# Kernel tuning notes

Hardware: AMD Instinct MI355X
Metric: run time of the kernel (lower is better)

Reference implementation:

```python
import jax, jax.numpy as jnp
import numpy as np
import math

BLKQ = 64
BLKK = 32
TOPK_FRAC = 0.1


def setup_inputs() -> dict:
    key = jax.random.key(0)
    k1, k2, k3, k4, k5 = jax.random.split(key, 5)
    B, L, H, D = 1, 8192, 16, 64
    q = jax.random.normal(k1, (B, L, H, D), jnp.float32)
    k = jax.random.normal(k2, (B, L, H, D), jnp.float32)
    v = jax.random.normal(k3, (B, L, H, D), jnp.float32)
    # proj_l initialized with nn.init.normal_ (std=1) in the original
    W_proj = jax.random.normal(k4, (D, D), jnp.float32)
    b_proj = jax.random.normal(k5, (D,), jnp.float32)
    return {"q": q, "k": k, "v": v, "W_proj": W_proj, "b_proj": b_proj}


def reference(q, k, v, W_proj, b_proj):
    B, L, H, D = q.shape
    lcm = BLKQ * BLKK // math.gcd(BLKQ, BLKK)
    L_pad = ((L + lcm - 1) // lcm) * lcm
    pad = L_pad - L
    scale = 1.0 / math.sqrt(D)

    # [B, L, H, D] -> [B, H, L_pad, D], zero padded (fused_transpose_pad)
    qt = jnp.transpose(q, (0, 2, 1, 3))
    kt = jnp.transpose(k, (0, 2, 1, 3))
    vt = jnp.transpose(v, (0, 2, 1, 3))
    if pad:
        pw = ((0, 0), (0, 0), (0, pad), (0, 0))
        qt_p = jnp.pad(qt, pw); kt_p = jnp.pad(kt, pw); vt_p = jnp.pad(vt, pw)
    else:
        qt_p, kt_p, vt_p = qt, kt, vt

    # key smoothing (SAGE): subtract per-(b,h) mean of padded k
    km = kt_p.mean(axis=-2, keepdims=True)          # [B, H, 1, D]
    kc = kt_p - km

    M = L_pad // BLKQ
    N = L_pad // BLKK
    # block pooling for routing scores
    pooled_q = qt_p.reshape(B, H, M, BLKQ, D).mean(axis=3)   # [B,H,M,D]
    pooled_k = kc.reshape(B, H, N, BLKK, D).mean(axis=3)     # [B,H,N,D]
    score = jnp.einsum('bhmd,bhnd->bhmn', pooled_q, pooled_k)

    T = min(N, int(TOPK_FRAC * N))                  # real_topk (static)
    _, idx = jax.lax.top_k(score, T)                # [B,H,M,T]
    lut = jnp.sort(idx, axis=-1)

    # gather selected key/value blocks: [B,H,M,T,BLKK,D]
    kb = kc.reshape(B, H, N, BLKK, D)
    vb = vt_p.reshape(B, H, N, BLKK, D)
    kg = jnp.take_along_axis(kb[:, :, None], lut[..., None, None], axis=3)
    vg = jnp.take_along_axis(vb[:, :, None], lut[..., None, None], axis=3)

    qb = qt_p.reshape(B, H, M, BLKQ, D)
    # block-sparse scores: [B,H,M,BLKQ,T,BLKK]
    s = jnp.einsum('bhmqd,bhmtkd->bhmqtk', qb, kg) * scale
    key_pos = lut[..., None] * BLKK + jnp.arange(BLKK)       # [B,H,M,T,BLKK]
    valid = key_pos < L
    s = jnp.where(valid[:, :, :, None, :, :], s, -jnp.inf)
    s = s.reshape(B, H, M, BLKQ, T * BLKK)
    p = jax.nn.softmax(s, axis=-1)
    o_s = jnp.einsum('bhmqn,bhmnd->bhmqd', p, vg.reshape(B, H, M, T * BLKK, D))
    o_s = o_s.reshape(B, H, L_pad, D)[:, :, :L]              # slice to seq_len

    # linear attention branch (softmax feature map over D)
    q_fm = jax.nn.softmax(qt_p[:, :, :L], axis=-1)
    k_fm = jax.nn.softmax(kt_p[:, :, :L], axis=-1)
    kvsum = jnp.einsum('bhld,bhle->bhde', k_fm, vt)          # [B,H,D,D]
    ksum = k_fm.sum(axis=-2)                                 # [B,H,D]
    denom = jnp.einsum('bhld,bhd->bhl', q_fm, ksum)[..., None] + 1e-6
    o_l = jnp.einsum('bhld,bhde->bhle', q_fm, kvsum) / denom
    o_l = o_l @ W_proj.T + b_proj                            # proj_l

    o = jnp.transpose(o_l + o_s, (0, 2, 1, 3))               # [B,L,H,D]
    return o
```

## Files before the change

### kernel.cpp

```cpp
#include <hip/hip_runtime.h>
#include <math.h>

#define SEQL 8192
#define NH 16
#define HD 1024
#define TSEL 25

#define OFF_KVPART 0
#define OFF_KSUM   262144
#define OFF_ZEND   263168
#define OFF_PK     263168
#define OFF_KWT    525312
#define OFF_KSWZ   558080

typedef __attribute__((ext_vector_type(8))) short bf16x8;
typedef __attribute__((ext_vector_type(4))) float f32x4;
typedef __attribute__((ext_vector_type(4))) unsigned u32x4;
typedef __attribute__((ext_vector_type(2))) unsigned u32x2;

static __device__ inline short f2bf(float f) {
    union { float f; unsigned u; } c; c.f = f;
    unsigned r = (c.u + 0x7FFFu + ((c.u >> 16) & 1u)) >> 16;
    return (short)r;
}
static __device__ inline bf16x8 cvt8(float4 a, float4 b) {
    bf16x8 r;
    r[0] = f2bf(a.x); r[1] = f2bf(a.y); r[2] = f2bf(a.z); r[3] = f2bf(a.w);
    r[4] = f2bf(b.x); r[5] = f2bf(b.y); r[6] = f2bf(b.z); r[7] = f2bf(b.w);
    return r;
}
static __device__ inline unsigned cvtpk(float a, float b) {
    unsigned r;
    asm("v_cvt_pk_bf16_f32 %0, %1, %2" : "=v"(r) : "v"(a), "v"(b));
    return r;
}
static __device__ inline float exp2a(float x) {
#if __has_builtin(__builtin_amdgcn_exp2f)
    return __builtin_amdgcn_exp2f(x);
#else
    float r; asm("v_exp_f32 %0, %1" : "=v"(r) : "v"(x)); return r;
#endif
}
#if __has_builtin(__builtin_amdgcn_permlane32_swap)
static __device__ inline unsigned xor32v(unsigned x, bool hi) {
    u32x2 r;
    {
        auto t = __builtin_amdgcn_permlane32_swap(x, x, false, false);
        r[0] = t[0]; r[1] = t[1];
    }
    return hi ? r[0] : r[1];
}
static __device__ inline unsigned xor16v(unsigned x, bool hi) {
    u32x2 r;
    {
        auto t = __builtin_amdgcn_permlane16_swap(x, x, false, false);
        r[0] = t[0]; r[1] = t[1];
    }
    return hi ? r[0] : r[1];
}
#else
static __device__ inline unsigned xor32v(unsigned x, bool hi) {
    unsigned a = x, b;
    asm("v_mov_b32 %0, %1" : "=v"(b) : "v"(x));
    asm("v_permlane32_swap_b32 %0, %1" : "+v"(a), "+v"(b));
    return hi ? a : b;
}
static __device__ inline unsigned xor16v(unsigned x, bool hi) {
    unsigned a = x, b;
    asm("v_mov_b32 %0, %1" : "=v"(b) : "v"(x));
    asm("v_permlane16_swap_b32 %0, %1" : "+v"(a), "+v"(b));
    return hi ? a : b;
}
#endif
static __device__ inline void load_lds16(const void* g, void* l) {
    __builtin_amdgcn_global_load_lds((const __attribute__((address_space(1))) unsigned int*)g,
                                     (__attribute__((address_space(3))) unsigned int*)l,
                                     16, 0, 0);
}

__global__ __launch_bounds__(256) void prep_lin(const float* __restrict__ k,
                                                const float* __restrict__ v,
                                                short* __restrict__ kswz,
                                                short* __restrict__ vswz,
                                                float* __restrict__ pk,
                                                float* __restrict__ kvpart,
                                                float* __restrict__ ksum) {
    __shared__ __align__(16) float kf[64][68];
    __shared__ __align__(16) float vv[64][68];
    __shared__ float pcol[2][4][64];
    int b = blockIdx.x;
    int h = b >> 6, sc = b & 63;
    int t = threadIdx.x;
    int lane = t & 63, w = t >> 6;
    int r32 = t >> 3, ch = t & 7;
    int d0 = (lane >> 4) * 4 + w * 16;
    int e0 = (lane & 15) * 4;
    float acc[16];
    #pragma unroll
    for (int i = 0; i < 16; i++) acc[i] = 0.f;
    float ks_acc = 0.f;

    const float* kb_ = k + (size_t)(sc * 128 + r32) * HD + h * 64 + ch * 8;
    const float* vb_ = v + (size_t)(sc * 128 + r32) * HD + h * 64 + ch * 8;
    float4 K0a = *(const float4*)kb_;
    float4 K0b = *(const float4*)(kb_ + 4);
    float4 K1a = *(const float4*)(kb_ + (size_t)32 * HD);
    float4 K1b = *(const float4*)(kb_ + (size_t)32 * HD + 4);
    float4 V0a = *(const float4*)vb_;
    float4 V0b = *(const float4*)(vb_ + 4);
    float4 V1a = *(const float4*)(vb_ + (size_t)32 * HD);
    float4 V1b = *(const float4*)(vb_ + (size_t)32 * HD + 4);

    #pragma unroll
    for (int ph = 0; ph < 2; ph++) {
        int n0 = sc * 4 + ph * 2;
        {
            *(float4*)&vv[r32][ch * 8]          = V0a;
            *(float4*)&vv[r32][ch * 8 + 4]      = V0b;
            *(float4*)&vv[32 + r32][ch * 8]     = V1a;
            *(float4*)&vv[32 + r32][ch * 8 + 4] = V1b;
        }
        {
            int f = r32 * 8 + (ch ^ (r32 & 7));
            *(bf16x8*)(kswz + (size_t)(h * 256 + n0) * 2048 + f * 8)     = cvt8(K0a, K0b);
            *(bf16x8*)(kswz + (size_t)(h * 256 + n0 + 1) * 2048 + f * 8) = cvt8(K1a, K1b);
        }
        {
            float s_[8] = { K0a.x, K0a.y, K0a.z, K0a.w, K0b.x, K0b.y, K0b.z, K0b.w };
            #pragma unroll
            for (int j = 0; j < 8; j++) {
                s_[j] += __shfl_xor(s_[j], 8, 64);
                s_[j] += __shfl_xor(s_[j], 16, 64);
                s_[j] += __shfl_xor(s_[j], 32, 64);
            }
            if (lane < 8) {
                #pragma unroll
                for (int j = 0; j < 8; j++) pcol[0][w][(t & 7) * 8 + j] = s_[j];
            }
            float s1_[8] = { K1a.x, K1a.y, K1a.z, K1a.w, K1b.x, K1b.y, K1b.z, K1b.w };
            #pragma unroll
            for (int j = 0; j < 8; j++) {
                s1_[j] += __shfl_xor(s1_[j], 8, 64);
                s1_[j] += __shfl_xor(s1_[j], 16, 64);
                s1_[j] += __shfl_xor(s1_[j], 32, 64);
            }
            if (lane < 8) {
                #pragma unroll
                for (int j = 0; j < 8; j++) pcol[1][w][(t & 7) * 8 + j] = s1_[j];
            }
        }
        {
            float mx = fmaxf(fmaxf(fmaxf(K0a.x, K0a.y), fmaxf(K0a.z, K0a.w)),
                             fmaxf(fmaxf(K0b.x, K0b.y), fmaxf(K0b.z, K0b.w)));
            mx = fmaxf(mx, __shfl_xor(mx, 1, 64));
            mx = fmaxf(mx, __shfl_xor(mx, 2, 64));
            mx = fmaxf(mx, __shfl_xor(mx, 4, 64));
            float4 Fa, Fb;
            Fa.x = __expf(K0a.x - mx); Fa.y = __expf(K0a.y - mx);
            Fa.z = __expf(K0a.z - mx); Fa.w = __expf(K0a.w - mx);
            Fb.x = __expf(K0b.x - mx); Fb.y = __expf(K0b.y - mx);
            Fb.z = __expf(K0b.z - mx); Fb.w = __expf(K0b.w - mx);
            float sm = (Fa.x + Fa.y + Fa.z + Fa.w) + (Fb.x + Fb.y + Fb.z + Fb.w);
            sm += __shfl_xor(sm, 1, 64);
            sm += __shfl_xor(sm, 2, 64);
            sm += __shfl_xor(sm, 4, 64);
            float inv = 1.f / sm;
            Fa.x *= inv; Fa.y *= inv; Fa.z *= inv; Fa.w *= inv;
            Fb.x *= inv; Fb.y *= inv; Fb.z *= inv; Fb.w *= inv;
            *(float4*)&kf[r32][ch * 8]     = Fa;
            *(float4*)&kf[r32][ch * 8 + 4] = Fb;
        }
        {
            float mx = fmaxf(fmaxf(fmaxf(K1a.x, K1a.y), fmaxf(K1a.z, K1a.w)),
                             fmaxf(fmaxf(K1b.x, K1b.y), fmaxf(K1b.z, K1b.w)));
            mx = fmaxf(mx, __shfl_xor(mx, 1, 64));
            mx = fmaxf(mx, __shfl_xor(mx, 2, 64));
            mx = fmaxf(mx, __shfl_xor(mx, 4, 64));
            float4 Fa, Fb;
            Fa.x = __expf(K1a.x - mx); Fa.y = __expf(K1a.y - mx);
            Fa.z = __expf(K1a.z - mx); Fa.w = __expf(K1a.w - mx);
            Fb.x = __expf(K1b.x - mx); Fb.y = __expf(K1b.y - mx);
            Fb.z = __expf(K1b.z - mx); Fb.w = __expf(K1b.w - mx);
            float sm = (Fa.x + Fa.y + Fa.z + Fa.w) + (Fb.x + Fb.y + Fb.z + Fb.w);
            sm += __shfl_xor(sm, 1, 64);
            sm += __shfl_xor(sm, 2, 64);
            sm += __shfl_xor(sm, 4, 64);
            float inv = 1.f / sm;
            Fa.x *= inv; Fa.y *= inv; Fa.z *= inv; Fa.w *= inv;
            Fb.x *= inv; Fb.y *= inv; Fb.z *= inv; Fb.w *= inv;
            *(float4*)&kf[32 + r32][ch * 8]     = Fa;
            *(float4*)&kf[32 + r32][ch * 8 + 4] = Fb;
        }
        if (ph < 1) {
            const float* kn = kb_ + (size_t)64 * HD;
            const float* vn = vb_ + (size_t)64 * HD;
            K0a = *(const float4*)kn;
            K0b = *(const float4*)(kn + 4);
            K1a = *(const float4*)(kn + (size_t)32 * HD);
            K1b = *(const float4*)(kn + (size_t)32 * HD + 4);
            V0a = *(const float4*)vn;
            V0b = *(const float4*)(vn + 4);
            V1a = *(const float4*)(vn + (size_t)32 * HD);
            V1b = *(const float4*)(vn + (size_t)32 * HD + 4);
        }
        __syncthreads();
        if (t < 128) {
            int s = t >> 6, d = t & 63;
            pk[(size_t)(h * 256 + n0 + s) * 64 + d] =
                (pcol[s][0][d] + pcol[s][1][d] + pcol[s][2][d] + pcol[s][3][d])
                * (1.f / 32.f);
        }
        {
            int c = w, d = lane;
            #pragma unroll
            for (int s = 0; s < 2; s++) {
                bf16x8 val;
                #pragma unroll
                for (int j = 0; j < 8; j++) val[j] = f2bf(vv[s * 32 + c * 8 + j][d]);
                int f = d * 4 + (c ^ ((d >> 1) & 3));
                *(bf16x8*)(vswz + (size_t)(h * 256 + n0 + s) * 2048 + f * 8) = val;
            }
        }
        #pragma unroll 8
        for (int l = 0; l < 64; l++) {
            float4 kd = *(const float4*)&kf[l][d0];
            float4 ve = *(const float4*)&vv[l][e0];
            acc[0]  += kd.x * ve.x; acc[1]  += kd.x * ve.y; acc[2]  += kd.x * ve.z; acc[3]  += kd.x * ve.w;
            acc[4]  += kd.y * ve.x; acc[5]  += kd.y * ve.y; acc[6]  += kd.y * ve.z; acc[7]  += kd.y * ve.w;
            acc[8]  += kd.z * ve.x; acc[9]  += kd.z * ve.y; acc[10] += kd.z * ve.z; acc[11] += kd.z * ve.w;
            acc[12] += kd.w * ve.x; acc[13] += kd.w * ve.y; acc[14] += kd.w * ve.z; acc[15] += kd.w * ve.w;
        }
        if (t < 64) {
            float s = 0.f;
            #pragma unroll 8
            for (int l = 0; l < 64; l++) s += kf[l][t];
            ks_acc += s;
        }
        __syncthreads();
    }
    float* dst = kvpart + ((size_t)(sc & 3) * 16 + h) * 4096;
    #pragma unroll
    for (int i = 0; i < 4; i++)
        #pragma unroll
        for (int j = 0; j < 4; j++)
            atomicAdd(&dst[(d0 + i) * 64 + e0 + j], acc[i * 4 + j]);
    if (t < 64) atomicAdd(&ksum[h * 64 + t], ks_acc);
}

__global__ __launch_bounds__(256) void kw_mul(const float* __restrict__ kvpart,
                                              const float* __restrict__ W,
                                              short* __restrict__ kwt) {
    __shared__ __align__(16) float kv[16][68];
    __shared__ __align__(16) float wsm[64][68];
    int h = blockIdx.x >> 2, dq = blockIdx.x & 3;
    int t = threadIdx.x;
    for (int i = t; i < 1024; i += 256) {
        int dl = i >> 6, e = i & 63;
        float s = 0.f;
        #pragma unroll
        for (int p = 0; p < 4; p++)
            s += kvpart[((size_t)p * 16 + h) * 4096 + (dq * 16 + dl) * 64 + e];
        kv[dl][e] = s;
    }
    for (int i = t; i < 4096; i += 256) wsm[i >> 6][i & 63] = W[i];
    __syncthreads();
    int lane = t & 63, wi = t >> 6;
    int dl = lane & 15;
    int db = wi * 16 + (lane >> 4) * 4;
    #pragma unroll
    for (int j = 0; j < 4; j++) {
        int dd = db + j;
        float a = 0.f;
        #pragma unroll
        for (int e4 = 0; e4 < 16; e4++) {
            float4 kq = *(const float4*)&kv[dl][e4 * 4];
            float4 wq = *(const float4*)&wsm[dd][e4 * 4];
            a += kq.x * wq.x + kq.y * wq.y + kq.z * wq.z + kq.w * wq.w;
        }
        kwt[(size_t)h * 4096 + dd * 64 + dq * 16 + dl] = f2bf(a);
    }
}

__global__ __launch_bounds__(256) void sparse_attn_mfma(const float* __restrict__ q,
                                                        const short* __restrict__ kswz,
                                                        const short* __restrict__ vswz,
                                                        const float* __restrict__ pk,
                                                        const short* __restrict__ kwt,
                                                        const float* __restrict__ ksum,
                                                        const float* __restrict__ bproj,
                                                        float* __restrict__ out) {
    __shared__ __align__(16) short Kb[3][2048];
    __shared__ __align__(16) short Vb[3][2048];
    __shared__ __align__(16) float pq_s[64];
    __shared__ __align__(16) float s_s[256];
    __shared__ int wcnt[4];
    __shared__ int lut_s[TSEL];

    int b = blockIdx.x;
    int x = b & 7, jj = b >> 3;
    int h = x * 2 + (jj >> 7);
    int m = jj & 127;
    int t = threadIdx.x;
    int lane = t & 63, w = t >> 6;
    int l15 = lane & 15, quad = lane >> 4;
    const bool b16 = (t & 16) != 0;
    const bool b32 = (t & 32) != 0;
    const bool beq = (b16 == b32);

    {
        load_lds16(kwt + (size_t)h * 4096 + t * 8, &Kb[1][t * 8]);
        load_lds16(kwt + (size_t)h * 4096 + 2048 + t * 8, &Vb[1][t * 8]);
    }

    if (t < 64) {
        const float* base = q + (size_t)m * 64 * HD + h * 64 + t;
        float s = 0.f;
        #pragma unroll 8
        for (int r = 0; r < 64; r++) s += base[(size_t)r * HD];
        pq_s[t] = s * (1.f / 64.f);
    }
    __syncthreads();
    {
        const float* kr = pk + ((size_t)h * 256 + t) * 64;
        double acc = 0.0;
        #pragma unroll 8
        for (int d = 0; d < 64; d++) acc += (double)pq_s[d] * (double)kr[d];
        float sc_ = (float)acc;
        s_s[t] = sc_;
        __syncthreads();
        int cnt = 0;
        float si = sc_;
        #pragma unroll 4
        for (int j4 = 0; j4 < 64; j4++) {
            float4 sv = *(const float4*)&s_s[j4 * 4];
            int j = j4 * 4;
            cnt += (sv.x > si) || (sv.x == si && (j + 0) < t);
            cnt += (sv.y > si) || (sv.y == si && (j + 1) < t);
            cnt += (sv.z > si) || (sv.z == si && (j + 2) < t);
            cnt += (sv.w > si) || (sv.w == si && (j + 3) < t);
        }
        bool sel = cnt < TSEL;
        unsigned long long bal = __ballot(sel);
        if (lane == 0) wcnt[w] = __popcll(bal);
        __syncthreads();
        if (sel) {
            int off = __popcll(bal & ((1ull << lane) - 1ull));
            for (int i = 0; i < w; i++) off += wcnt[i];
            lut_s[off] = t;
        }
        __syncthreads();
    }

    {
        size_t base = (size_t)(h * 256 + lut_s[0]) * 2048;
        load_lds16(kswz + base + t * 8, &Kb[0][t * 8]);
        load_lds16(vswz + base + t * 8, &Vb[0][t * 8]);
    }

    const float* qrow = q + (size_t)(m * 64 + w * 16 + l15) * HD + h * 64;
    float4 x0 = *(const float4*)(qrow + quad * 8);
    float4 x1 = *(const float4*)(qrow + quad * 8 + 4);
    float4 x2 = *(const float4*)(qrow + 32 + quad * 8);
    float4 x3 = *(const float4*)(qrow + 32 + quad * 8 + 4);
    bf16x8 qa[2];
    qa[0] = cvt8(x0, x1);
    qa[1] = cvt8(x2, x3);

    float mx = fmaxf(fmaxf(fmaxf(x0.x, x0.y), fmaxf(x0.z, x0.w)),
                     fmaxf(fmaxf(x1.x, x1.y), fmaxf(x1.z, x1.w)));
    mx = fmaxf(mx, fmaxf(fmaxf(fmaxf(x2.x, x2.y), fmaxf(x2.z, x2.w)),
                         fmaxf(fmaxf(x3.x, x3.y), fmaxf(x3.z, x3.w))));
    mx = fmaxf(mx, __shfl_xor(mx, 16, 64));
    mx = fmaxf(mx, __shfl_xor(mx, 32, 64));
    x0.x = __expf(x0.x - mx); x0.y = __expf(x0.y - mx); x0.z = __expf(x0.z - mx); x0.w = __expf(x0.w - mx);
    x1.x = __expf(x1.x - mx); x1.y = __expf(x1.y - mx); x1.z = __expf(x1.z - mx); x1.w = __expf(x1.w - mx);
    x2.x = __expf(x2.x - mx); x2.y = __expf(x2.y - mx); x2.z = __expf(x2.z - mx); x2.w = __expf(x2.w - mx);
    x3.x = __expf(x3.x - mx); x3.y = __expf(x3.y - mx); x3.z = __expf(x3.z - mx); x3.w = __expf(x3.w - mx);
    float sm = (x0.x + x0.y + x0.z + x0.w) + (x1.x + x1.y + x1.z + x1.w)
             + (x2.x + x2.y + x2.z + x2.w) + (x3.x + x3.y + x3.z + x3.w);
    sm += __shfl_xor(sm, 16, 64);
    sm += __shfl_xor(sm, 32, 64);
    float qsc = 1.f / sm;
    float4 ka0 = *(const float4*)(ksum + h * 64 + quad * 8);
    float4 ka1 = *(const float4*)(ksum + h * 64 + quad * 8 + 4);
    float4 ka2 = *(const float4*)(ksum + h * 64 + 32 + quad * 8);
    float4 ka3 = *(const float4*)(ksum + h * 64 + 32 + quad * 8 + 4);
    float dq = x0.x * ka0.x + x0.y * ka0.y + x0.z * ka0.z + x0.w * ka0.w
             + x1.x * ka1.x + x1.y * ka1.y + x1.z * ka1.z + x1.w * ka1.w
             + x2.x * ka2.x + x2.y * ka2.y + x2.z * ka2.z + x2.w * ka2.w
             + x3.x * ka3.x + x3.y * ka3.y + x3.z * ka3.z + x3.w * ka3.w;
    dq += __shfl_xor(dq, 16, 64);
    dq += __shfl_xor(dq, 32, 64);
    float invd = 1.f / (dq * qsc + 1e-6f);
    x0.x *= qsc; x0.y *= qsc; x0.z *= qsc; x0.w *= qsc;
    x1.x *= qsc; x1.y *= qsc; x1.z *= qsc; x1.w *= qsc;
    x2.x *= qsc; x2.y *= qsc; x2.z *= qsc; x2.w *= qsc;
    x3.x *= qsc; x3.y *= qsc; x3.z *= qsc; x3.w *= qsc;
    bf16x8 qf[2];
    qf[0] = cvt8(x0, x1);
    qf[1] = cvt8(x2, x3);

    __syncthreads();

    f32x4 Ol[4];
    #pragma unroll
    for (int dt = 0; dt < 4; dt++) Ol[dt] = (f32x4){0.f, 0.f, 0.f, 0.f};
    __builtin_amdgcn_s_setprio(1);
    #pragma unroll
    for (int dt = 0; dt < 4; dt++) {
        #pragma unroll
        for (int kc = 0; kc < 2; kc++) {
            int flat = (dt * 16 + l15) * 64 + kc * 32 + quad * 8;
            bf16x8 a = (dt < 2) ? *(const bf16x8*)&Kb[1][flat]
                                : *(const bf16x8*)&Vb[1][flat - 2048];
            Ol[dt] = __builtin_amdgcn_mfma_f32_16x16x32_bf16(a, qf[kc], Ol[dt], 0, 0, 0);
        }
    }
    __builtin_amdgcn_s_setprio(0);

    __syncthreads();
    {
        size_t base = (size_t)(h * 256 + lut_s[1]) * 2048;
        load_lds16(kswz + base + t * 8, &Kb[1][t * 8]);
        load_lds16(vswz + base + t * 8, &Vb[1][t * 8]);
    }

    f32x4 O[4];
    #pragma unroll
    for (int dt = 0; dt < 4; dt++) O[dt] = (f32x4){0.f, 0.f, 0.f, 0.f};
    float l_loc = 0.f;
    const f32x4 z = (f32x4){0.f, 0.f, 0.f, 0.f};
    const float EC = 1.44269504f * 0.125f;

    int bc = 0;
    for (int ti = 0; ti < TSEL; ti++) {
        if (ti > 0) {
            if (ti < TSEL - 1) asm volatile("s_waitcnt vmcnt(2)" ::: "memory");
            else               asm volatile("s_waitcnt vmcnt(0)" ::: "memory");
            __builtin_amdgcn_s_barrier();
            __builtin_amdgcn_sched_barrier(0);
        }
        if (ti + 2 < TSEL) {
            int bs = bc ? bc - 1 : 2;
            size_t base = (size_t)(h * 256 + lut_s[ti + 2]) * 2048;
            load_lds16(kswz + base + t * 8, &Kb[bs][t * 8]);
            load_lds16(vswz + base + t * 8, &Vb[bs][t * 8]);
        }
        int r0 = l15, r1 = 16 + l15;
        bf16x8 a00 = *(const bf16x8*)&Kb[bc][(r0 * 8 + (quad ^ (r0 & 7))) * 8];
        bf16x8 a01 = *(const bf16x8*)&Kb[bc][(r0 * 8 + ((4 + quad) ^ (r0 & 7))) * 8];
        bf16x8 a10 = *(const bf16x8*)&Kb[bc][(r1 * 8 + (quad ^ (r1 & 7))) * 8];
        bf16x8 a11 = *(const bf16x8*)&Kb[bc][(r1 * 8 + ((4 + quad) ^ (r1 & 7))) * 8];
        bf16x8 va[4];
        #pragma unroll
        for (int dt = 0; dt < 4; dt++) {
            int d = dt * 16 + l15;
            va[dt] = *(const bf16x8*)&Vb[bc][(d * 4 + (quad ^ ((d >> 1) & 3))) * 8];
        }
        __builtin_amdgcn_s_setprio(1);
        f32x4 s0 = __builtin_amdgcn_mfma_f32_16x16x32_bf16(a00, qa[0], z, 0, 0, 0);
        s0 = __builtin_amdgcn_mfma_f32_16x16x32_bf16(a01, qa[1], s0, 0, 0, 0);
        f32x4 s1 = __builtin_amdgcn_mfma_f32_16x16x32_bf16(a10, qa[0], z, 0, 0, 0);
        s1 = __builtin_amdgcn_mfma_f32_16x16x32_bf16(a11, qa[1], s1, 0, 0, 0);
        __builtin_amdgcn_s_setprio(0);

        float p0[4], p1[4];
        #pragma unroll
        for (int r = 0; r < 4; r++) {
            p0[r] = exp2a(s0[r] * EC);
            p1[r] = exp2a(s1[r] * EC);
        }
        l_loc += ((p0[0] + p0[1]) + (p0[2] + p0[3])) + ((p1[0] + p1[1]) + (p1[2] + p1[3]));

        unsigned c0 = cvtpk(p0[0], p0[1]);
        unsigned c1 = cvtpk(p0[2], p0[3]);
        unsigned c2 = cvtpk(p1[0], p1[1]);
        unsigned c3 = cvtpk(p1[2], p1[3]);
        unsigned d0_ = xor32v(c0, b32), d1_ = xor32v(c1, b32);
        unsigned d2_ = xor32v(c2, b32), d3_ = xor32v(c3, b32);
        unsigned cc0 = b32 ? c2 : c0,  cc1 = b32 ? c3 : c1;
        unsigned dd0 = b32 ? d2_ : d0_, dd1 = b32 ? d3_ : d1_;
        unsigned sw0 = beq ? cc0 : dd0, sw1 = beq ? cc1 : dd1;
        unsigned t0_ = beq ? dd0 : cc0, t1_ = beq ? dd1 : cc1;
        unsigned rv0 = xor16v(t0_, b16), rv1 = xor16v(t1_, b16);
        u32x4 pw;
        pw[0] = b16 ? rv0 : sw0; pw[1] = b16 ? rv1 : sw1;
        pw[2] = b16 ? sw0 : rv0; pw[3] = b16 ? sw1 : rv1;
        bf16x8 pb = __builtin_bit_cast(bf16x8, pw);

        __builtin_amdgcn_s_setprio(1);
        #pragma unroll
        for (int dt = 0; dt < 4; dt++)
            O[dt] = __builtin_amdgcn_mfma_f32_16x16x32_bf16(va[dt], pb, O[dt], 0, 0, 0);
        __builtin_amdgcn_s_setprio(0);

        bc++; if (bc == 3) bc = 0;
    }

    l_loc += __shfl_xor(l_loc, 16, 64);
    l_loc += __shfl_xor(l_loc, 32, 64);
    float inv = 1.f / l_loc;
    float* dst = out + (size_t)(m * 64 + w * 16 + l15) * HD + h * 64;
    #pragma unroll
    for (int dt = 0; dt < 4; dt++) {
        float4 bv = *(const float4*)(bproj + dt * 16 + quad * 4);
        float4 o;
        o.x = O[dt][0] * inv + Ol[dt][0] * invd + bv.x;
        o.y = O[dt][1] * inv + Ol[dt][1] * invd + bv.y;
        o.z = O[dt][2] * inv + Ol[dt][2] * invd + bv.z;
        o.w = O[dt][3] * inv + Ol[dt][3] * invd + bv.w;
        *(float4*)(dst + dt * 16 + quad * 4) = o;
    }
}

extern "C" void kernel_launch(void* const* d_in, const int* in_sizes, int n_in,
                              void* d_out, int out_size, void* d_ws, size_t ws_size,
                              hipStream_t stream) {
    const float* q  = (const float*)d_in[0];
    const float* k  = (const float*)d_in[1];
    const float* v  = (const float*)d_in[2];
    const float* W  = (const float*)d_in[3];
    const float* bp = (const float*)d_in[4];
    float* out = (float*)d_out;
    float* ws = (float*)d_ws;

    float* kvpart = ws + OFF_KVPART;
    float* ksum   = ws + OFF_KSUM;
    float* pk     = ws + OFF_PK;
    short* kwt    = (short*)(ws + OFF_KWT);
    short* kswz   = (short*)(ws + OFF_KSWZ);
    short* vswz   = kswz + (size_t)16 * 256 * 2048;

    hipMemsetAsync(ws, 0, OFF_ZEND * sizeof(float), stream);
    prep_lin<<<1024, 256, 0, stream>>>(k, v, kswz, vswz, pk, kvpart, ksum);
    kw_mul<<<64, 256, 0, stream>>>(kvpart, W, kwt);
    sparse_attn_mfma<<<2048, 256, 0, stream>>>(q, kswz, vswz, pk, kwt, ksum, bp, out);
}
```

Before: 294.8 us.

## Move block routing top-k into the middle kernel alongside kw_mul

Moves the pooled-query computation, score dot products and top-k selection out of the sparse attention kernel into the previously tiny kw_mul launch, which now also runs 2048 routing blocks that write a LUT to workspace. The attention kernel then only loads the precomputed LUT, so its prologue becomes shorter and the routing work runs in parallel with the 64 kw blocks rather than serialising inside each attention block. The cost is an extra global round trip for the LUT and a re-read of q in the middle kernel.

```diff
diff --git a/kernel.cpp b/kernel.cpp
--- a/kernel.cpp
+++ b/kernel.cpp
@@ -12,6 +12,7 @@
 #define OFF_PK     263168
 #define OFF_KWT    525312
 #define OFF_KSWZ   558080
+#define OFF_LUT    8946688
 
 typedef __attribute__((ext_vector_type(8))) short bf16x8;
 typedef __attribute__((ext_vector_type(4))) float f32x4;
@@ -247,53 +248,98 @@
     if (t < 64) atomicAdd(&ksum[h * 64 + t], ks_acc);
 }
 
-__global__ __launch_bounds__(256) void kw_mul(const float* __restrict__ kvpart,
-                                              const float* __restrict__ W,
-                                              short* __restrict__ kwt) {
+__global__ __launch_bounds__(256) void mid_kw_topk(const float* __restrict__ kvpart,
+                                                   const float* __restrict__ W,
+                                                   short* __restrict__ kwt,
+                                                   const float* __restrict__ q,
+                                                   const float* __restrict__ pk,
+                                                   int* __restrict__ lut) {
     __shared__ __align__(16) float kv[16][68];
     __shared__ __align__(16) float wsm[64][68];
-    int h = blockIdx.x >> 2, dq = blockIdx.x & 3;
+    __shared__ __align__(16) float pq_s[64];
+    __shared__ __align__(16) float s_s[256];
+    __shared__ int wcnt[4];
+    int bb = blockIdx.x;
     int t = threadIdx.x;
-    for (int i = t; i < 1024; i += 256) {
-        int dl = i >> 6, e = i & 63;
-        float s = 0.f;
+    if (bb < 64) {
+        int h = bb >> 2, dq = bb & 3;
+        for (int i = t; i < 1024; i += 256) {
+            int dl = i >> 6, e = i & 63;
+            float s = 0.f;
+            #pragma unroll
+            for (int p = 0; p < 4; p++)
+                s += kvpart[((size_t)p * 16 + h) * 4096 + (dq * 16 + dl) * 64 + e];
+            kv[dl][e] = s;
+        }
+        for (int i = t; i < 4096; i += 256) wsm[i >> 6][i & 63] = W[i];
+        __syncthreads();
+        int lane = t & 63, wi = t >> 6;
+        int dl = lane & 15;
+        int db = wi * 16 + (lane >> 4) * 4;
         #pragma unroll
-        for (int p = 0; p < 4; p++)
-            s += kvpart[((size_t)p * 16 + h) * 4096 + (dq * 16 + dl) * 64 + e];
-        kv[dl][e] = s;
-    }
-    for (int i = t; i < 4096; i += 256) wsm[i >> 6][i & 63] = W[i];
-    __syncthreads();
-    int lane = t & 63, wi = t >> 6;
-    int dl = lane & 15;
-    int db = wi * 16 + (lane >> 4) * 4;
-    #pragma unroll
-    for (int j = 0; j < 4; j++) {
-        int dd = db + j;
-        float a = 0.f;
-        #pragma unroll
-        for (int e4 = 0; e4 < 16; e4++) {
-            float4 kq = *(const float4*)&kv[dl][e4 * 4];
-            float4 wq = *(const float4*)&wsm[dd][e4 * 4];
-            a += kq.x * wq.x + kq.y * wq.y + kq.z * wq.z + kq.w * wq.w;
-        }
-        kwt[(size_t)h * 4096 + dd * 64 + dq * 16 + dl] = f2bf(a);
+        for (int j = 0; j < 4; j++) {
+            int dd = db + j;
+            float a = 0.f;
+            #pragma unroll
+            for (int e4 = 0; e4 < 16; e4++) {
+                float4 kq = *(const float4*)&kv[dl][e4 * 4];
+                float4 wq = *(const float4*)&wsm[dd][e4 * 4];
+                a += kq.x * wq.x + kq.y * wq.y + kq.z * wq.z + kq.w * wq.w;
+            }
+            kwt[(size_t)h * 4096 + dd * 64 + dq * 16 + dl] = f2bf(a);
+        }
+    } else {
+        int b = bb - 64;
+        int h = b >> 7, m = b & 127;
+        int lane = t & 63, w = t >> 6;
+        if (t < 64) {
+            const float* base = q + (size_t)m * 64 * HD + h * 64 + t;
+            float s = 0.f;
+            #pragma unroll 8
+            for (int r = 0; r < 64; r++) s += base[(size_t)r * HD];
+            pq_s[t] = s * (1.f / 64.f);
+        }
+        __syncthreads();
+        const float* kr = pk + ((size_t)h * 256 + t) * 64;
+        double acc = 0.0;
+        #pragma unroll 8
+        for (int d = 0; d < 64; d++) acc += (double)pq_s[d] * (double)kr[d];
+        float sc = (float)acc;
+        s_s[t] = sc;
+        __syncthreads();
+        int cnt = 0;
+        float si = sc;
+        #pragma unroll 4
+        for (int j4 = 0; j4 < 64; j4++) {
+            float4 sv = *(const float4*)&s_s[j4 * 4];
+            int j = j4 * 4;
+            cnt += (sv.x > si) || (sv.x == si && (j + 0) < t);
+            cnt += (sv.y > si) || (sv.y == si && (j + 1) < t);
+            cnt += (sv.z > si) || (sv.z == si && (j + 2) < t);
+            cnt += (sv.w > si) || (sv.w == si && (j + 3) < t);
+        }
+        bool sel = cnt < TSEL;
+        unsigned long long bal = __ballot(sel);
+        if (lane == 0) wcnt[w] = __popcll(bal);
+        __syncthreads();
+        if (sel) {
+            int off = __popcll(bal & ((1ull << lane) - 1ull));
+            for (int i = 0; i < w; i++) off += wcnt[i];
+            lut[(size_t)b * TSEL + off] = t;
+        }
     }
 }
 
 __global__ __launch_bounds__(256) void sparse_attn_mfma(const float* __restrict__ q,
                                                         const short* __restrict__ kswz,
                                                         const short* __restrict__ vswz,
-                                                        const float* __restrict__ pk,
+                                                        const int* __restrict__ lut,
                                                         const short* __restrict__ kwt,
                                                         const float* __restrict__ ksum,
                                                         const float* __restrict__ bproj,
                                                         float* __restrict__ out) {
     __shared__ __align__(16) short Kb[3][2048];
     __shared__ __align__(16) short Vb[3][2048];
-    __shared__ __align__(16) float pq_s[64];
-    __shared__ __align__(16) float s_s[256];
-    __shared__ int wcnt[4];
     __shared__ int lut_s[TSEL];
 
     int b = blockIdx.x;
@@ -307,54 +353,15 @@
     const bool b32 = (t & 32) != 0;
     const bool beq = (b16 == b32);
 
-    {
-        load_lds16(kwt + (size_t)h * 4096 + t * 8, &Kb[1][t * 8]);
-        load_lds16(kwt + (size_t)h * 4096 + 2048 + t * 8, &Vb[1][t * 8]);
-    }
-
-    if (t < 64) {
-        const float* base = q + (size_t)m * 64 * HD + h * 64 + t;
-        float s = 0.f;
-        #pragma unroll 8
-        for (int r = 0; r < 64; r++) s += base[(size_t)r * HD];
-        pq_s[t] = s * (1.f / 64.f);
-    }
+    if (t < TSEL) lut_s[t] = lut[(size_t)(h * 128 + m) * TSEL + t];
     __syncthreads();
-    {
-        const float* kr = pk + ((size_t)h * 256 + t) * 64;
-        double acc = 0.0;
-        #pragma unroll 8
-        for (int d = 0; d < 64; d++) acc += (double)pq_s[d] * (double)kr[d];
-        float sc_ = (float)acc;
-        s_s[t] = sc_;
-        __syncthreads();
-        int cnt = 0;
-        float si = sc_;
-        #pragma unroll 4
-        for (int j4 = 0; j4 < 64; j4++) {
-            float4 sv = *(const float4*)&s_s[j4 * 4];
-            int j = j4 * 4;
-            cnt += (sv.x > si) || (sv.x == si && (j + 0) < t);
-            cnt += (sv.y > si) || (sv.y == si && (j + 1) < t);
-            cnt += (sv.z > si) || (sv.z == si && (j + 2) < t);
-            cnt += (sv.w > si) || (sv.w == si && (j + 3) < t);
-        }
-        bool sel = cnt < TSEL;
-        unsigned long long bal = __ballot(sel);
-        if (lane == 0) wcnt[w] = __popcll(bal);
-        __syncthreads();
-        if (sel) {
-            int off = __popcll(bal & ((1ull << lane) - 1ull));
-            for (int i = 0; i < w; i++) off += wcnt[i];
-            lut_s[off] = t;
-        }
-        __syncthreads();
-    }
 
     {
         size_t base = (size_t)(h * 256 + lut_s[0]) * 2048;
         load_lds16(kswz + base + t * 8, &Kb[0][t * 8]);
         load_lds16(vswz + base + t * 8, &Vb[0][t * 8]);
+        load_lds16(kwt + (size_t)h * 4096 + t * 8, &Kb[1][t * 8]);
+        load_lds16(kwt + (size_t)h * 4096 + 2048 + t * 8, &Vb[1][t * 8]);
     }
 
     const float* qrow = q + (size_t)(m * 64 + w * 16 + l15) * HD + h * 64;
@@ -530,9 +537,10 @@
     short* kwt    = (short*)(ws + OFF_KWT);
     short* kswz   = (short*)(ws + OFF_KSWZ);
     short* vswz   = kswz + (size_t)16 * 256 * 2048;
+    int*   lut    = (int*)(ws + OFF_LUT);
 
     hipMemsetAsync(ws, 0, OFF_ZEND * sizeof(float), stream);
     prep_lin<<<1024, 256, 0, stream>>>(k, v, kswz, vswz, pk, kvpart, ksum);
-    kw_mul<<<64, 256, 0, stream>>>(kvpart, W, kwt);
-    sparse_attn_mfma<<<2048, 256, 0, stream>>>(q, kswz, vswz, pk, kwt, ksum, bp, out);
-}
+    mid_kw_topk<<<2112, 256, 0, stream>>>(kvpart, W, kwt, q, pk, lut);
+    sparse_attn_mfma<<<2048, 256, 0, stream>>>(q, kswz, vswz, lut, kwt, ksum, bp, out);
+}
```

Result: no change. 294.5 us (-0.1%).
